# Kernel tuning notes

Hardware: AMD Instinct MI355X
Metric: run time of the kernel (lower is better)

Reference implementation:

```python
import jax, jax.numpy as jnp
import numpy as np

COEF = 0.1   # cfg.MODEL.SS.COEF
P, U, V, F = 8, 256, 256, 256 * 49  # pairs, u-proposals, v-proposals, ROI feat dim (256*7*7)


def setup_inputs() -> dict:
    key = jax.random.key(0)
    k1, k2 = jax.random.split(key)
    feat_u = jax.random.normal(k1, (P, U, F), dtype=jnp.float32)
    feat_v = jax.random.normal(k2, (P, V, F), dtype=jnp.float32)
    return {"feat_u": feat_u, "feat_v": feat_v}


def reference(feat_u, feat_v):
    # Pairwise squared L2 distance without materializing the O(U*V*F) expanded tensor:
    # ||u - v||^2 = ||u||^2 + ||v||^2 - 2 u.v
    uu = jnp.sum(feat_u * feat_u, axis=-1)                 # [P, U]
    vv = jnp.sum(feat_v * feat_v, axis=-1)                 # [P, V]
    uv = jnp.einsum('puf,pvf->puv', feat_u, feat_v)        # [P, U, V]
    dist = (uu[:, :, None] + vv[:, None, :] - 2.0 * uv) * COEF
    # Original applies softmax directly to the (positive) distances along v.
    score = jax.nn.softmax(dist, axis=-1)                  # [P, U, V]
    # neg_fea = score @ feat_v  (soft-kNN aggregation)
    neg_fea = jnp.einsum('puv,pvf->puf', score, feat_v)    # [P, U, F]
    pos_fea = feat_u.reshape(-1, F)                        # [P*U, F]
    # forward returns torch.cat([pos_fea, neg_fea], 0)
    return jnp.concatenate([pos_fea, neg_fea.reshape(-1, F)], axis=0)
```

## Files before the change

### kernel.cpp

```cpp
#include <hip/hip_runtime.h>
#include <cstdint>
#include <cstddef>

#define P_DIM 8
#define U_DIM 256
#define V_DIM 256
#define F_DIM 12544

typedef __attribute__((ext_vector_type(8))) short short8;
typedef __attribute__((ext_vector_type(8))) _Float16 half8;
typedef __attribute__((ext_vector_type(4))) float f32x4;

#define MFMA16B(a, b, c) __builtin_amdgcn_mfma_f32_16x16x32_bf16((a), (b), (c), 0, 0, 0)
#define MFMA16H(a, b, c) __builtin_amdgcn_mfma_f32_16x16x32_f16((a), (b), (c), 0, 0, 0)

__device__ __forceinline__ unsigned short f2bf(float x) {
  unsigned u = __builtin_bit_cast(unsigned, x);
  u += 0x7FFFu + ((u >> 16) & 1u);
  return (unsigned short)(u >> 16);
}

__device__ __forceinline__ uint4 cvt8h(float4 a, float4 b) {
  float x[8] = {a.x, a.y, a.z, a.w, b.x, b.y, b.z, b.w};
  unsigned w[4];
  #pragma unroll
  for (int i = 0; i < 4; ++i) {
    unsigned short lo = __builtin_bit_cast(unsigned short, (_Float16)x[2 * i]);
    unsigned short hi = __builtin_bit_cast(unsigned short, (_Float16)x[2 * i + 1]);
    w[i] = (unsigned)lo | ((unsigned)hi << 16);
  }
  return uint4{w[0], w[1], w[2], w[3]};
}

__global__ __launch_bounds__(256) void prep_fv(const float* __restrict__ fv,
                                               unsigned short* __restrict__ fvT,
                                               float* __restrict__ vvpart) {
  __shared__ unsigned short tile[64][65];
  __shared__ float vvp[64];
  int f0 = blockIdx.x * 64, v0 = blockIdx.y * 64, p = blockIdx.z;
  const float* src = fv + (size_t)p * V_DIM * F_DIM;
  int t = threadIdx.x;
  #pragma unroll
  for (int i = 0; i < 4; ++i) {
    int g = t + i * 256;
    int r = g >> 4;
    int c4 = (g & 15) * 4;
    float4 x = *(const float4*)(src + (size_t)(v0 + r) * F_DIM + f0 + c4);
    tile[r][c4 + 0] = f2bf(x.x);
    tile[r][c4 + 1] = f2bf(x.y);
    tile[r][c4 + 2] = f2bf(x.z);
    tile[r][c4 + 3] = f2bf(x.w);
    float ps = x.x * x.x + x.y * x.y + x.z * x.z + x.w * x.w;
    ps += __shfl_xor(ps, 1); ps += __shfl_xor(ps, 2);
    ps += __shfl_xor(ps, 4); ps += __shfl_xor(ps, 8);
    if ((t & 15) == 0) vvp[r] = ps;
  }
  __syncthreads();
  if (t < 64)
    vvpart[((size_t)blockIdx.x * P_DIM + p) * V_DIM + v0 + t] = vvp[t];
  unsigned short* dst = fvT + (size_t)p * F_DIM * V_DIM;
  #pragma unroll
  for (int i = 0; i < 2; ++i) {
    int g = t + i * 256;
    int f = g >> 3;
    int v8 = (g & 7) * 8;
    short8 o;
    #pragma unroll
    for (int j = 0; j < 8; ++j) o[j] = (short)tile[v8 + j][f];
    *(short8*)(dst + (size_t)(f0 + f) * V_DIM + v0 + v8) = o;
  }
}

__global__ __launch_bounds__(256) void vv_reduce(const float* __restrict__ vvpart,
                                                 float* __restrict__ vv) {
  int p = blockIdx.x >> 2;
  int vb = (blockIdx.x & 3) * 64;
  int vl = threadIdx.x & 63;
  int v = vb + vl;
  int js = threadIdx.x >> 6;
  float s = 0.f;
  for (int j = js; j < F_DIM / 64; j += 4)
    s += vvpart[((size_t)j * P_DIM + p) * V_DIM + v];
  __shared__ float red[4][64];
  red[js][vl] = s;
  __syncthreads();
  if (threadIdx.x < 64)
    vv[p * V_DIM + v] = red[0][vl] + red[1][vl] + red[2][vl] + red[3][vl];
}

__global__ __launch_bounds__(256) void copy_kernel(const float4* __restrict__ src,
                                                   float4* __restrict__ dst, int n4) {
  for (int i = blockIdx.x * 256 + threadIdx.x; i < n4; i += gridDim.x * 256)
    dst[i] = src[i];
}

__global__ __launch_bounds__(256, 2) void uv_gemm(const float* __restrict__ fu,
                                                  const float* __restrict__ fv,
                                                  float* __restrict__ part,
                                                  int splitk, int chunk) {
  int nwg = gridDim.x;
  int q = nwg >> 3, r = nwg & 7;
  int xcd = blockIdx.x & 7, ofs = blockIdx.x >> 3;
  int wgid = (xcd < r ? xcd * (q + 1) : r * (q + 1) + (xcd - r) * q) + ofs;
  int nt = wgid & 1, mt = (wgid >> 1) & 1, p = (wgid >> 2) & 7, ks = wgid >> 5;

  const float* A = fu + ((size_t)p * U_DIM + mt * 128) * F_DIM;
  const float* B = fv + ((size_t)p * V_DIM + nt * 128) * F_DIM;
  int k0 = ks * chunk;
  int nkt = chunk >> 6;

  __shared__ short AS[128 * 64], BS[128 * 64];
  char* Ap = (char*)AS; char* Bp = (char*)BS;

  int tid = threadIdx.x, lane = tid & 63, wid = tid >> 6;
  int wm = wid >> 1, wn = wid & 1;
  int rl = lane & 15;
  f32x4 acc[4][4] = {};
  float4 ra[8], rb[8];

#define LOAD_TILE(kg)                                                          \
  do {                                                                         \
    _Pragma("unroll") for (int j = 0; j < 4; ++j) {                            \
      int g = tid + j * 256; int rr = g >> 3; int c8 = (g & 7) * 8;            \
      const float* s = A + (size_t)rr * F_DIM + (kg) + c8;                     \
      ra[2 * j] = *(const float4*)s; ra[2 * j + 1] = *(const float4*)(s + 4);  \
      const float* s2 = B + (size_t)rr * F_DIM + (kg) + c8;                    \
      rb[2 * j] = *(const float4*)s2; rb[2 * j + 1] = *(const float4*)(s2 + 4);\
    }                                                                          \
  } while (0)

  LOAD_TILE(k0);
  for (int kt = 0; kt < nkt; ++kt) {
    #pragma unroll
    for (int j = 0; j < 4; ++j) {
      int g = tid + j * 256;
      int rr = g >> 3;
      int off = (rr * 128 + (g & 7) * 16) ^ ((rr & 7) << 4);
      *(uint4*)(Ap + off) = cvt8h(ra[2 * j], ra[2 * j + 1]);
      *(uint4*)(Bp + off) = cvt8h(rb[2 * j], rb[2 * j + 1]);
    }
    __syncthreads();
    if (kt + 1 < nkt) LOAD_TILE(k0 + (kt + 1) * 64);
    #pragma unroll
    for (int kk = 0; kk < 2; ++kk) {
      int kbyte = kk * 64 + (lane >> 4) * 16;
      half8 ah[4], bh[4];
      #pragma unroll
      for (int m = 0; m < 4; ++m) {
        int row = wm * 64 + m * 16 + rl;
        int off = (row * 128 + kbyte) ^ ((row & 7) << 4);
        ah[m] = *(const half8*)(Ap + off);
      }
      #pragma unroll
      for (int n = 0; n < 4; ++n) {
        int row = wn * 64 + n * 16 + rl;
        int off = (row * 128 + kbyte) ^ ((row & 7) << 4);
        bh[n] = *(const half8*)(Bp + off);
      }
      #pragma unroll
      for (int m = 0; m < 4; ++m)
        #pragma unroll
        for (int n = 0; n < 4; ++n)
          acc[m][n] = MFMA16H(ah[m], bh[n], acc[m][n]);
    }
    __syncthreads();
  }
#undef LOAD_TILE
  float* dst = part + ((size_t)ks * P_DIM + p) * U_DIM * V_DIM;
  int rq = lane >> 4;
  #pragma unroll
  for (int m = 0; m < 4; ++m)
    #pragma unroll
    for (int n = 0; n < 4; ++n)
      #pragma unroll
      for (int i = 0; i < 4; ++i) {
        int u = mt * 128 + wm * 64 + m * 16 + rq * 4 + i;
        int v = nt * 128 + wn * 64 + n * 16 + rl;
        dst[(size_t)u * V_DIM + v] = acc[m][n][i];
      }
}

__global__ __launch_bounds__(256) void reduce_softmax(const float* __restrict__ part,
                                                      const float* __restrict__ vv,
                                                      unsigned short* __restrict__ score,
                                                      int splitk) {
  int u = blockIdx.x & 255, p = blockIdx.x >> 8;
  int v = threadIdx.x;
  size_t base = ((size_t)p * U_DIM + u) * V_DIM + v;
  float s = 0.f;
  for (int k = 0; k < splitk; ++k)
    s += part[(size_t)k * (P_DIM * U_DIM * V_DIM) + base];
  float logit = 0.1f * vv[p * V_DIM + v] - 0.2f * s;
  float m = logit;
  #pragma unroll
  for (int off = 32; off >= 1; off >>= 1) m = fmaxf(m, __shfl_xor(m, off));
  __shared__ float red[4], red2[4];
  int lane = v & 63, wid = v >> 6;
  if (lane == 0) red[wid] = m;
  __syncthreads();
  m = fmaxf(fmaxf(red[0], red[1]), fmaxf(red[2], red[3]));
  float e = __expf(logit - m);
  float tsum = e;
  #pragma unroll
  for (int off = 32; off >= 1; off >>= 1) tsum += __shfl_xor(tsum, off);
  if (lane == 0) red2[wid] = tsum;
  __syncthreads();
  tsum = red2[0] + red2[1] + red2[2] + red2[3];
  score[base] = f2bf(e / tsum);
}

__global__ __launch_bounds__(512, 1) void pv_gemm(const unsigned short* __restrict__ score,
                                                  const unsigned short* __restrict__ fvT,
                                                  float* __restrict__ outneg) {
  int bx = blockIdx.x;
  int p = blockIdx.y;
  int n0 = bx * 128;
  const unsigned short* Sc = score + (size_t)p * U_DIM * V_DIM;
  const unsigned short* Bt = fvT + ((size_t)p * F_DIM + n0) * V_DIM;
  __shared__ short Bs[128 * 256];
  char* Bsp = (char*)Bs;
  int tid = threadIdx.x, lane = tid & 63, wid = tid >> 6;
  int rl = lane & 15, rq = lane >> 4;

  short8 a[2][8];
  #pragma unroll
  for (int m = 0; m < 2; ++m)
    #pragma unroll
    for (int k = 0; k < 8; ++k)
      a[m][k] = *(const short8*)(Sc + (size_t)(wid * 32 + m * 16 + rl) * V_DIM
                                 + k * 32 + rq * 8);

  {
    int row = tid >> 2;
    int seg = (tid & 3) * 128;
    const char* src = (const char*)(Bt + (size_t)row * V_DIM) + seg;
    char* dstrow = Bsp + row * 512;
    int swz = (row & 7) << 4;
    #pragma unroll
    for (int j = 0; j < 8; ++j) {
      uint4 x = *(const uint4*)(src + j * 16);
      *(uint4*)(dstrow + ((seg + j * 16) ^ swz)) = x;
    }
  }
  __syncthreads();

  f32x4 acc[2][8] = {};
  #pragma unroll
  for (int k = 0; k < 8; ++k) {
    #pragma unroll
    for (int n = 0; n < 8; ++n) {
      int row = n * 16 + rl;
      half8 bdummy;
      short8 b = *(const short8*)(Bsp + row * 512
                                  + ((k * 64 + rq * 16) ^ ((row & 7) << 4)));
      acc[0][n] = MFMA16B(a[0][k], b, acc[0][n]);
      acc[1][n] = MFMA16B(a[1][k], b, acc[1][n]);
      (void)bdummy;
    }
  }

  float* dst = outneg + (size_t)p * U_DIM * F_DIM;
  #pragma unroll
  for (int m = 0; m < 2; ++m)
    #pragma unroll
    for (int n = 0; n < 8; ++n)
      #pragma unroll
      for (int i = 0; i < 4; ++i) {
        int u = wid * 32 + m * 16 + rq * 4 + i;
        int f = n0 + n * 16 + rl;
        dst[(size_t)u * F_DIM + f] = acc[m][n][i];
      }
}

extern "C" void kernel_launch(void* const* d_in, const int* in_sizes, int n_in,
                              void* d_out, int out_size, void* d_ws, size_t ws_size,
                              hipStream_t stream) {
  const float* fu = (const float*)d_in[0];
  const float* fv = (const float*)d_in[1];
  float* out = (float*)d_out;
  char* ws = (char*)d_ws;

  float* vv = (float*)ws;
  unsigned short* score = (unsigned short*)(ws + 8192);
  unsigned short* fvT = (unsigned short*)(ws + 8192 + 1048576);
  size_t vvpartBase = 8192 + 1048576 + (size_t)P_DIM * F_DIM * V_DIM * 2;
  float* vvpart = (float*)(ws + vvpartBase);
  size_t partBase = vvpartBase + (size_t)(F_DIM / 64) * P_DIM * V_DIM * 4;
  float* part = (float*)(ws + partBase);

  const size_t puv4 = (size_t)P_DIM * U_DIM * V_DIM * 4;
  int splitk = 1;
  const int cands[5] = {14, 7, 4, 2, 1};
  for (int i = 0; i < 5; ++i) {
    if (partBase + (size_t)cands[i] * puv4 <= ws_size) { splitk = cands[i]; break; }
  }
  int chunk = F_DIM / splitk;

  prep_fv<<<dim3(F_DIM / 64, V_DIM / 64, P_DIM), 256, 0, stream>>>(fv, fvT, vvpart);
  vv_reduce<<<P_DIM * 4, 256, 0, stream>>>(vvpart, vv);
  int n4 = (P_DIM * U_DIM * F_DIM) / 4;
  copy_kernel<<<2048, 256, 0, stream>>>((const float4*)fu, (float4*)out, n4);
  uv_gemm<<<splitk * 32, 256, 0, stream>>>(fu, fv, part, splitk, chunk);
  reduce_softmax<<<P_DIM * U_DIM, 256, 0, stream>>>(part, vv, score, splitk);
  pv_gemm<<<dim3(F_DIM / 128, P_DIM), 512, 0, stream>>>(
      score, fvT, out + (size_t)P_DIM * U_DIM * F_DIM);
}
```

Measured before the change: 205.1 us.

## Pre-convert inputs to fp16 and stream GEMM tiles via direct global-to-LDS loads

Each fp32 input is now converted to fp16 once. feat_v is converted in prep_fv and feat_u in the copy kernel, and both are written to workspace buffers. The UV GEMM then loads fp16 tiles straight into LDS with global_load_lds, replacing the register-staged fp32 loads and the in-loop conversion. The split-K candidates gain 28, and pv_gemm is retiled to 256-thread blocks over a 64x128 tile with async LDS loads. The trade is extra global writes and reads for the fp16 copies, and the loss of the register prefetch overlap in the UV loop.

```diff
diff --git a/kernel.cpp b/kernel.cpp
--- a/kernel.cpp
+++ b/kernel.cpp
@@ -14,31 +14,29 @@
 #define MFMA16B(a, b, c) __builtin_amdgcn_mfma_f32_16x16x32_bf16((a), (b), (c), 0, 0, 0)
 #define MFMA16H(a, b, c) __builtin_amdgcn_mfma_f32_16x16x32_f16((a), (b), (c), 0, 0, 0)
 
+#define GLOAD16(gsrc, ldsbase)                                                \
+  __builtin_amdgcn_global_load_lds(                                           \
+      (const __attribute__((address_space(1))) void*)(gsrc),                  \
+      (__attribute__((address_space(3))) void*)(ldsbase), 16, 0, 0)
+
 __device__ __forceinline__ unsigned short f2bf(float x) {
   unsigned u = __builtin_bit_cast(unsigned, x);
   u += 0x7FFFu + ((u >> 16) & 1u);
   return (unsigned short)(u >> 16);
 }
-
-__device__ __forceinline__ uint4 cvt8h(float4 a, float4 b) {
-  float x[8] = {a.x, a.y, a.z, a.w, b.x, b.y, b.z, b.w};
-  unsigned w[4];
-  #pragma unroll
-  for (int i = 0; i < 4; ++i) {
-    unsigned short lo = __builtin_bit_cast(unsigned short, (_Float16)x[2 * i]);
-    unsigned short hi = __builtin_bit_cast(unsigned short, (_Float16)x[2 * i + 1]);
-    w[i] = (unsigned)lo | ((unsigned)hi << 16);
-  }
-  return uint4{w[0], w[1], w[2], w[3]};
+__device__ __forceinline__ unsigned short f2h(float x) {
+  return __builtin_bit_cast(unsigned short, (_Float16)x);
 }
 
 __global__ __launch_bounds__(256) void prep_fv(const float* __restrict__ fv,
                                                unsigned short* __restrict__ fvT,
+                                               unsigned short* __restrict__ fvH,
                                                float* __restrict__ vvpart) {
   __shared__ unsigned short tile[64][65];
   __shared__ float vvp[64];
   int f0 = blockIdx.x * 64, v0 = blockIdx.y * 64, p = blockIdx.z;
   const float* src = fv + (size_t)p * V_DIM * F_DIM;
+  unsigned short* dstH = fvH + (size_t)p * V_DIM * F_DIM;
   int t = threadIdx.x;
   #pragma unroll
   for (int i = 0; i < 4; ++i) {
@@ -50,6 +48,9 @@
     tile[r][c4 + 1] = f2bf(x.y);
     tile[r][c4 + 2] = f2bf(x.z);
     tile[r][c4 + 3] = f2bf(x.w);
+    ushort4 h;
+    h.x = f2h(x.x); h.y = f2h(x.y); h.z = f2h(x.z); h.w = f2h(x.w);
+    *(ushort4*)(dstH + (size_t)(v0 + r) * F_DIM + f0 + c4) = h;
     float ps = x.x * x.x + x.y * x.y + x.z * x.z + x.w * x.w;
     ps += __shfl_xor(ps, 1); ps += __shfl_xor(ps, 2);
     ps += __shfl_xor(ps, 4); ps += __shfl_xor(ps, 8);
@@ -88,14 +89,20 @@
     vv[p * V_DIM + v] = red[0][vl] + red[1][vl] + red[2][vl] + red[3][vl];
 }
 
-__global__ __launch_bounds__(256) void copy_kernel(const float4* __restrict__ src,
-                                                   float4* __restrict__ dst, int n4) {
-  for (int i = blockIdx.x * 256 + threadIdx.x; i < n4; i += gridDim.x * 256)
-    dst[i] = src[i];
-}
-
-__global__ __launch_bounds__(256, 2) void uv_gemm(const float* __restrict__ fu,
-                                                  const float* __restrict__ fv,
+__global__ __launch_bounds__(256) void copy_fu(const float4* __restrict__ src,
+                                               float4* __restrict__ dst,
+                                               ushort4* __restrict__ fuH, int n4) {
+  for (int i = blockIdx.x * 256 + threadIdx.x; i < n4; i += gridDim.x * 256) {
+    float4 x = src[i];
+    dst[i] = x;
+    ushort4 h;
+    h.x = f2h(x.x); h.y = f2h(x.y); h.z = f2h(x.z); h.w = f2h(x.w);
+    fuH[i] = h;
+  }
+}
+
+__global__ __launch_bounds__(256, 2) void uv_gemm(const unsigned short* __restrict__ fuH,
+                                                  const unsigned short* __restrict__ fvH,
                                                   float* __restrict__ part,
                                                   int splitk, int chunk) {
   int nwg = gridDim.x;
@@ -104,8 +111,8 @@
   int wgid = (xcd < r ? xcd * (q + 1) : r * (q + 1) + (xcd - r) * q) + ofs;
   int nt = wgid & 1, mt = (wgid >> 1) & 1, p = (wgid >> 2) & 7, ks = wgid >> 5;
 
-  const float* A = fu + ((size_t)p * U_DIM + mt * 128) * F_DIM;
-  const float* B = fv + ((size_t)p * V_DIM + nt * 128) * F_DIM;
+  const unsigned short* A = fuH + ((size_t)p * U_DIM + mt * 128) * F_DIM;
+  const unsigned short* B = fvH + ((size_t)p * V_DIM + nt * 128) * F_DIM;
   int k0 = ks * chunk;
   int nkt = chunk >> 6;
 
@@ -116,31 +123,20 @@
   int wm = wid >> 1, wn = wid & 1;
   int rl = lane & 15;
   f32x4 acc[4][4] = {};
-  float4 ra[8], rb[8];
-
-#define LOAD_TILE(kg)                                                          \
-  do {                                                                         \
-    _Pragma("unroll") for (int j = 0; j < 4; ++j) {                            \
-      int g = tid + j * 256; int rr = g >> 3; int c8 = (g & 7) * 8;            \
-      const float* s = A + (size_t)rr * F_DIM + (kg) + c8;                     \
-      ra[2 * j] = *(const float4*)s; ra[2 * j + 1] = *(const float4*)(s + 4);  \
-      const float* s2 = B + (size_t)rr * F_DIM + (kg) + c8;                    \
-      rb[2 * j] = *(const float4*)s2; rb[2 * j + 1] = *(const float4*)(s2 + 4);\
-    }                                                                          \
-  } while (0)
-
-  LOAD_TILE(k0);
+
   for (int kt = 0; kt < nkt; ++kt) {
+    int kg = k0 + kt * 64;
     #pragma unroll
     for (int j = 0; j < 4; ++j) {
       int g = tid + j * 256;
-      int rr = g >> 3;
-      int off = (rr * 128 + (g & 7) * 16) ^ ((rr & 7) << 4);
-      *(uint4*)(Ap + off) = cvt8h(ra[2 * j], ra[2 * j + 1]);
-      *(uint4*)(Bp + off) = cvt8h(rb[2 * j], rb[2 * j + 1]);
+      int row = g >> 3;
+      int c = g & 7;
+      int sc = c ^ (row & 7);
+      int ldsbase = (wid * 64 + j * 256) * 16;
+      GLOAD16(A + (size_t)row * F_DIM + kg + sc * 8, Ap + ldsbase);
+      GLOAD16(B + (size_t)row * F_DIM + kg + sc * 8, Bp + ldsbase);
     }
     __syncthreads();
-    if (kt + 1 < nkt) LOAD_TILE(k0 + (kt + 1) * 64);
     #pragma unroll
     for (int kk = 0; kk < 2; ++kk) {
       int kbyte = kk * 64 + (lane >> 4) * 16;
@@ -165,7 +161,6 @@
     }
     __syncthreads();
   }
-#undef LOAD_TILE
   float* dst = part + ((size_t)ks * P_DIM + p) * U_DIM * V_DIM;
   int rq = lane >> 4;
   #pragma unroll
@@ -209,19 +204,30 @@
   score[base] = f2bf(e / tsum);
 }
 
-__global__ __launch_bounds__(512, 1) void pv_gemm(const unsigned short* __restrict__ score,
+__global__ __launch_bounds__(256, 2) void pv_gemm(const unsigned short* __restrict__ score,
                                                   const unsigned short* __restrict__ fvT,
                                                   float* __restrict__ outneg) {
   int bx = blockIdx.x;
-  int p = blockIdx.y;
-  int n0 = bx * 128;
-  const unsigned short* Sc = score + (size_t)p * U_DIM * V_DIM;
+  int my = blockIdx.y;
+  int p = blockIdx.z;
+  int n0 = bx * 64;
+  const unsigned short* Sc = score + ((size_t)p * U_DIM + my * 128) * V_DIM;
   const unsigned short* Bt = fvT + ((size_t)p * F_DIM + n0) * V_DIM;
-  __shared__ short Bs[128 * 256];
+  __shared__ short Bs[64 * 256];
   char* Bsp = (char*)Bs;
   int tid = threadIdx.x, lane = tid & 63, wid = tid >> 6;
   int rl = lane & 15, rq = lane >> 4;
 
+  #pragma unroll
+  for (int j = 0; j < 8; ++j) {
+    int g = tid + j * 256;
+    int row = g >> 5;
+    int c = g & 31;
+    int sc = c ^ (row & 7);
+    int ldsbase = (wid * 64 + j * 256) * 16;
+    GLOAD16(Bt + (size_t)row * V_DIM + sc * 8, Bsp + ldsbase);
+  }
+
   short8 a[2][8];
   #pragma unroll
   for (int m = 0; m < 2; ++m)
@@ -229,41 +235,26 @@
     for (int k = 0; k < 8; ++k)
       a[m][k] = *(const short8*)(Sc + (size_t)(wid * 32 + m * 16 + rl) * V_DIM
                                  + k * 32 + rq * 8);
-
-  {
-    int row = tid >> 2;
-    int seg = (tid & 3) * 128;
-    const char* src = (const char*)(Bt + (size_t)row * V_DIM) + seg;
-    char* dstrow = Bsp + row * 512;
-    int swz = (row & 7) << 4;
-    #pragma unroll
-    for (int j = 0; j < 8; ++j) {
-      uint4 x = *(const uint4*)(src + j * 16);
-      *(uint4*)(dstrow + ((seg + j * 16) ^ swz)) = x;
-    }
-  }
-  __syncthreads();
-
-  f32x4 acc[2][8] = {};
+  __syncthreads();
+
+  f32x4 acc[2][4] = {};
   #pragma unroll
   for (int k = 0; k < 8; ++k) {
     #pragma unroll
-    for (int n = 0; n < 8; ++n) {
+    for (int n = 0; n < 4; ++n) {
       int row = n * 16 + rl;
-      half8 bdummy;
       short8 b = *(const short8*)(Bsp + row * 512
                                   + ((k * 64 + rq * 16) ^ ((row & 7) << 4)));
       acc[0][n] = MFMA16B(a[0][k], b, acc[0][n]);
       acc[1][n] = MFMA16B(a[1][k], b, acc[1][n]);
-      (void)bdummy;
     }
   }
 
-  float* dst = outneg + (size_t)p * U_DIM * F_DIM;
+  float* dst = outneg + ((size_t)p * U_DIM + my * 128) * F_DIM;
   #pragma unroll
   for (int m = 0; m < 2; ++m)
     #pragma unroll
-    for (int n = 0; n < 8; ++n)
+    for (int n = 0; n < 4; ++n)
       #pragma unroll
       for (int i = 0; i < 4; ++i) {
         int u = wid * 32 + m * 16 + rq * 4 + i;
@@ -280,28 +271,33 @@
   float* out = (float*)d_out;
   char* ws = (char*)d_ws;
 
+  const size_t HVF = (size_t)P_DIM * F_DIM * V_DIM * 2;
   float* vv = (float*)ws;
   unsigned short* score = (unsigned short*)(ws + 8192);
   unsigned short* fvT = (unsigned short*)(ws + 8192 + 1048576);
-  size_t vvpartBase = 8192 + 1048576 + (size_t)P_DIM * F_DIM * V_DIM * 2;
+  unsigned short* fuH = (unsigned short*)(ws + 8192 + 1048576 + HVF);
+  unsigned short* fvH = (unsigned short*)(ws + 8192 + 1048576 + 2 * HVF);
+  size_t vvpartBase = 8192 + 1048576 + 3 * HVF;
   float* vvpart = (float*)(ws + vvpartBase);
   size_t partBase = vvpartBase + (size_t)(F_DIM / 64) * P_DIM * V_DIM * 4;
   float* part = (float*)(ws + partBase);
 
   const size_t puv4 = (size_t)P_DIM * U_DIM * V_DIM * 4;
   int splitk = 1;
-  const int cands[5] = {14, 7, 4, 2, 1};
-  for (int i = 0; i < 5; ++i) {
+  const int cands[6] = {28, 14, 7, 4, 2, 1};
+  for (int i = 0; i < 6; ++i) {
     if (partBase + (size_t)cands[i] * puv4 <= ws_size) { splitk = cands[i]; break; }
   }
   int chunk = F_DIM / splitk;
 
-  prep_fv<<<dim3(F_DIM / 64, V_DIM / 64, P_DIM), 256, 0, stream>>>(fv, fvT, vvpart);
+  prep_fv<<<dim3(F_DIM / 64, V_DIM / 64, P_DIM), 256, 0, stream>>>(fv, fvT, fvH,
+                                                                   vvpart);
   vv_reduce<<<P_DIM * 4, 256, 0, stream>>>(vvpart, vv);
   int n4 = (P_DIM * U_DIM * F_DIM) / 4;
-  copy_kernel<<<2048, 256, 0, stream>>>((const float4*)fu, (float4*)out, n4);
-  uv_gemm<<<splitk * 32, 256, 0, stream>>>(fu, fv, part, splitk, chunk);
+  copy_fu<<<2048, 256, 0, stream>>>((const float4*)fu, (float4*)out,
+                                    (ushort4*)fuH, n4);
+  uv_gemm<<<splitk * 32, 256, 0, stream>>>(fuH, fvH, part, splitk, chunk);
   reduce_softmax<<<P_DIM * U_DIM, 256, 0, stream>>>(part, vv, score, splitk);
-  pv_gemm<<<dim3(F_DIM / 128, P_DIM), 512, 0, stream>>>(
+  pv_gemm<<<dim3(F_DIM / 64, 2, P_DIM), 256, 0, stream>>>(
       score, fvT, out + (size_t)P_DIM * U_DIM * F_DIM);
 }
```

After: 208.9 us. About the same (+1.9%).

## Retile pv_gemm into smaller blocks and load B tile via direct global-to-LDS

Applied to the files above, without the earlier changes.

The PV GEMM now uses 256-thread blocks, each covering 128 U rows and 64 F columns, instead of 512-thread blocks covering all 256 U rows and 128 F columns. This quadruples the grid and allows two blocks per CU. The B-tile fill now uses global_load_lds to write straight into LDS, keeping the XOR swizzle, instead of going through registers. The intent is better latency hiding and occupancy, at the cost of reading each fvT tile twice, once per U-half.

```diff
diff --git a/kernel.cpp b/kernel.cpp
--- a/kernel.cpp
+++ b/kernel.cpp
@@ -13,6 +13,11 @@
 
 #define MFMA16B(a, b, c) __builtin_amdgcn_mfma_f32_16x16x32_bf16((a), (b), (c), 0, 0, 0)
 #define MFMA16H(a, b, c) __builtin_amdgcn_mfma_f32_16x16x32_f16((a), (b), (c), 0, 0, 0)
+
+#define GLOAD16(gsrc, ldsbase)                                                \
+  __builtin_amdgcn_global_load_lds(                                           \
+      (const __attribute__((address_space(1))) void*)(gsrc),                  \
+      (__attribute__((address_space(3))) void*)(ldsbase), 16, 0, 0)
 
 __device__ __forceinline__ unsigned short f2bf(float x) {
   unsigned u = __builtin_bit_cast(unsigned, x);
@@ -209,19 +214,30 @@
   score[base] = f2bf(e / tsum);
 }
 
-__global__ __launch_bounds__(512, 1) void pv_gemm(const unsigned short* __restrict__ score,
+__global__ __launch_bounds__(256, 2) void pv_gemm(const unsigned short* __restrict__ score,
                                                   const unsigned short* __restrict__ fvT,
                                                   float* __restrict__ outneg) {
-  int bx = blockIdx.x;
-  int p = blockIdx.y;
-  int n0 = bx * 128;
-  const unsigned short* Sc = score + (size_t)p * U_DIM * V_DIM;
+  int my = blockIdx.x;
+  int bx = blockIdx.y;
+  int p = blockIdx.z;
+  int n0 = bx * 64;
+  const unsigned short* Sc = score + ((size_t)p * U_DIM + my * 128) * V_DIM;
   const unsigned short* Bt = fvT + ((size_t)p * F_DIM + n0) * V_DIM;
-  __shared__ short Bs[128 * 256];
+  __shared__ short Bs[64 * 256];
   char* Bsp = (char*)Bs;
   int tid = threadIdx.x, lane = tid & 63, wid = tid >> 6;
   int rl = lane & 15, rq = lane >> 4;
 
+  #pragma unroll
+  for (int j = 0; j < 8; ++j) {
+    int g = tid + j * 256;
+    int row = g >> 5;
+    int c = g & 31;
+    int sc = c ^ (row & 7);
+    int ldsbase = (wid * 64 + j * 256) * 16;
+    GLOAD16(Bt + (size_t)row * V_DIM + sc * 8, Bsp + ldsbase);
+  }
+
   short8 a[2][8];
   #pragma unroll
   for (int m = 0; m < 2; ++m)
@@ -229,41 +245,26 @@
     for (int k = 0; k < 8; ++k)
       a[m][k] = *(const short8*)(Sc + (size_t)(wid * 32 + m * 16 + rl) * V_DIM
                                  + k * 32 + rq * 8);
-
-  {
-    int row = tid >> 2;
-    int seg = (tid & 3) * 128;
-    const char* src = (const char*)(Bt + (size_t)row * V_DIM) + seg;
-    char* dstrow = Bsp + row * 512;
-    int swz = (row & 7) << 4;
-    #pragma unroll
-    for (int j = 0; j < 8; ++j) {
-      uint4 x = *(const uint4*)(src + j * 16);
-      *(uint4*)(dstrow + ((seg + j * 16) ^ swz)) = x;
-    }
-  }
-  __syncthreads();
-
-  f32x4 acc[2][8] = {};
+  __syncthreads();
+
+  f32x4 acc[2][4] = {};
   #pragma unroll
   for (int k = 0; k < 8; ++k) {
     #pragma unroll
-    for (int n = 0; n < 8; ++n) {
+    for (int n = 0; n < 4; ++n) {
       int row = n * 16 + rl;
-      half8 bdummy;
       short8 b = *(const short8*)(Bsp + row * 512
                                   + ((k * 64 + rq * 16) ^ ((row & 7) << 4)));
       acc[0][n] = MFMA16B(a[0][k], b, acc[0][n]);
       acc[1][n] = MFMA16B(a[1][k], b, acc[1][n]);
-      (void)bdummy;
     }
   }
 
-  float* dst = outneg + (size_t)p * U_DIM * F_DIM;
+  float* dst = outneg + ((size_t)p * U_DIM + my * 128) * F_DIM;
   #pragma unroll
   for (int m = 0; m < 2; ++m)
     #pragma unroll
-    for (int n = 0; n < 8; ++n)
+    for (int n = 0; n < 4; ++n)
       #pragma unroll
       for (int i = 0; i < 4; ++i) {
         int u = wid * 32 + m * 16 + rq * 4 + i;
@@ -280,10 +281,11 @@
   float* out = (float*)d_out;
   char* ws = (char*)d_ws;
 
+  const size_t HVF = (size_t)P_DIM * F_DIM * V_DIM * 2;
   float* vv = (float*)ws;
   unsigned short* score = (unsigned short*)(ws + 8192);
   unsigned short* fvT = (unsigned short*)(ws + 8192 + 1048576);
-  size_t vvpartBase = 8192 + 1048576 + (size_t)P_DIM * F_DIM * V_DIM * 2;
+  size_t vvpartBase = 8192 + 1048576 + HVF;
   float* vvpart = (float*)(ws + vvpartBase);
   size_t partBase = vvpartBase + (size_t)(F_DIM / 64) * P_DIM * V_DIM * 4;
   float* part = (float*)(ws + partBase);
@@ -302,6 +304,6 @@
   copy_kernel<<<2048, 256, 0, stream>>>((const float4*)fu, (float4*)out, n4);
   uv_gemm<<<splitk * 32, 256, 0, stream>>>(fu, fv, part, splitk, chunk);
   reduce_softmax<<<P_DIM * U_DIM, 256, 0, stream>>>(part, vv, score, splitk);
-  pv_gemm<<<dim3(F_DIM / 128, P_DIM), 512, 0, stream>>>(
+  pv_gemm<<<dim3(2, F_DIM / 64, P_DIM), 256, 0, stream>>>(
       score, fvT, out + (size_t)P_DIM * U_DIM * F_DIM);
 }
```

Result: no change. 206.1 us (+0.5%).
